# Optimization experiments

Measured on AMD Instinct MI355X. Metric: run time of the kernel, lower is better.

Reference implementation:

```python
import jax, jax.numpy as jnp
import numpy as np

N_NODES = 100000
N_EDGES = 1600000
EMB_DIM = 128
BN_EPS = 1e-5


def setup_inputs() -> dict:
    key = jax.random.key(0)
    k = jax.random.split(key, 5)
    x = jax.random.normal(k[0], (N_NODES, EMB_DIM), dtype=jnp.float32)
    src = jax.random.randint(k[1], (N_EDGES,), 0, N_NODES)
    dst = jax.random.randint(k[2], (N_EDGES,), 0, N_NODES)
    W = jax.random.normal(k[3], (EMB_DIM, EMB_DIM), dtype=jnp.float32) / np.float32(np.sqrt(EMB_DIM))
    b = jnp.zeros((EMB_DIM,), dtype=jnp.float32)
    gamma = jnp.ones((EMB_DIM,), dtype=jnp.float32)
    beta = jnp.zeros((EMB_DIM,), dtype=jnp.float32)
    return {"x": x, "src": src, "dst": dst, "W": W, "b": b, "gamma": gamma, "beta": beta}


def reference(x, src, dst, W, b, gamma, beta):
    n = x.shape[0]
    ones = jnp.ones(src.shape, dtype=x.dtype)
    # DGL GraphConv norm='both': degrees clamped to min 1
    deg_out = jnp.maximum(jax.ops.segment_sum(ones, src, num_segments=n), 1.0)
    deg_in = jnp.maximum(jax.ops.segment_sum(ones, dst, num_segments=n), 1.0)
    norm_src = jax.lax.rsqrt(deg_out)  # [N]
    norm_dst = jax.lax.rsqrt(deg_in)   # [N]
    # W applied before aggregation (in_feats == out_feats path in DGL)
    h = (x * norm_src[:, None]) @ W                              # [N, D]
    agg = jax.ops.segment_sum(h[src], dst, num_segments=n)       # SpMM gather/scatter, [N, D]
    h = agg * norm_dst[:, None] + b                              # [N, D]
    # BatchNorm1d over nodes (training-mode batch stats, biased variance)
    mean = jnp.mean(h, axis=0)
    var = jnp.var(h, axis=0)
    h = (h - mean) * jax.lax.rsqrt(var + BN_EPS) * gamma + beta
    h = jax.nn.relu(h)
    # dropout: identity in eval-mode reference
    return h + x  # residual
```

## Files before the change

### kernel.cpp

```cpp
#include <hip/hip_runtime.h>
#include <hip/hip_bf16.h>

#define NN 100000
#define NE 1600000
#define D  128
#define BN_EPS 1e-5f

#define CB  782
#define NC  256
#define EPC (NE / NC)
#define NSLICE  2
#define SLICESZ 61600
#define SW      (SLICESZ / 4)
#define SCH     256
#define EPH (NE / SCH)

#define GB   ((NN + 63) / 64)
#define SMB  ((NSLICE * SW + 255) / 256)

typedef __attribute__((ext_vector_type(8))) short bf16x8;
typedef __attribute__((ext_vector_type(4))) float f32x4;

#define WLD 136

static __device__ __forceinline__ ushort f2bf(float f) {
    __hip_bfloat16 b = __float2bfloat16(f);
    return *reinterpret_cast<ushort*>(&b);
}
static __device__ __forceinline__ float bflo(unsigned v) {
    return __uint_as_float((v & 0xffffu) << 16);
}
static __device__ __forceinline__ float bfhi(unsigned v) {
    return __uint_as_float(v & 0xffff0000u);
}

__global__ __launch_bounds__(256) void k_front(const int* __restrict__ src,
                                               const int* __restrict__ dst,
                                               const float* __restrict__ W,
                                               ushort* __restrict__ WT,
                                               int* __restrict__ SP,
                                               int* __restrict__ P,
                                               float* __restrict__ stats) {
    __shared__ int hist[SW];
    __shared__ int dh[CB];
    const int t = threadIdx.x;
    const int s = blockIdx.x >> 8;
    const int c = blockIdx.x & 255;
    for (int i = t; i < SW; i += 256) hist[i] = 0;
    for (int i = t; i < CB; i += 256) dh[i] = 0;
    __syncthreads();

    const int lo = s * SLICESZ;
    const int base = c * EPH;
    for (int i = t; i < EPH; i += 256) {
        int k = src[base + i] - lo;
        if ((unsigned)k < (unsigned)SLICESZ)
            atomicAdd(&hist[k >> 2], 1 << ((k & 3) * 8));
    }
    if (s == 0) {
        for (int i = t; i < EPH; i += 256)
            atomicAdd(&dh[dst[base + i] >> 7], 1);
    }
    __syncthreads();

    int* outS = SP + (size_t)blockIdx.x * SW;
    for (int i = t; i < SW; i += 256) outS[i] = hist[i];
    if (s == 0)
        for (int i = t; i < CB; i += 256) P[i * NC + c] = dh[i];
    if (s == 1 && c < 64) {
        int i = c * 256 + t;
        int n = i >> 7, k2 = i & 127;
        WT[i] = f2bf(W[k2 * D + n]);
    }
    if (s == 1 && c == 64) stats[t] = 0.0f;
}

__global__ __launch_bounds__(256) void k_mid(int* __restrict__ P,
                                             int* __restrict__ bintotal,
                                             const int* __restrict__ SP,
                                             float* __restrict__ degout) {
    const int t = threadIdx.x;
    if (blockIdx.x < CB) {
        __shared__ int sh[NC];
        const int b = blockIdx.x;
        const int v = P[b * NC + t];
        sh[t] = v;
        __syncthreads();
        for (int off = 1; off < NC; off <<= 1) {
            int u = (t >= off) ? sh[t - off] : 0;
            __syncthreads();
            sh[t] += u;
            __syncthreads();
        }
        P[b * NC + t] = sh[t] - v;
        if (t == NC - 1) bintotal[b] = sh[t];
    } else {
        int w = (blockIdx.x - CB) * 256 + t;
        if (w >= NSLICE * SW) return;
        const int s = w / SW, wi = w - s * SW;
        const int n0 = s * SLICESZ + wi * 4;
        if (n0 >= NN) return;
        const int* col = SP + (size_t)s * SCH * SW + wi;
        int b0 = 0, b1 = 0, b2 = 0, b3 = 0;
#pragma unroll 8
        for (int c = 0; c < SCH; ++c) {
            unsigned v = (unsigned)col[(size_t)c * SW];
            b0 += v & 0xFF;
            b1 += (v >> 8) & 0xFF;
            b2 += (v >> 16) & 0xFF;
            b3 += (v >> 24);
        }
        degout[n0] = (float)b0;
        if (n0 + 1 < NN) degout[n0 + 1] = (float)b1;
        if (n0 + 2 < NN) degout[n0 + 2] = (float)b2;
        if (n0 + 3 < NN) degout[n0 + 3] = (float)b3;
    }
}

__global__ __launch_bounds__(256) void k_csg(const float* __restrict__ x,
                                             const float* __restrict__ degout,
                                             const ushort* __restrict__ WT,
                                             ushort* __restrict__ h,
                                             const int* __restrict__ dst,
                                             const int* __restrict__ src,
                                             const int* __restrict__ P,
                                             const int* __restrict__ bintotal,
                                             int* __restrict__ binbase,
                                             int* __restrict__ sedge) {
    __shared__ ushort Wl[D * WLD];
    __shared__ int part[256];
    __shared__ int bb[CB];
    __shared__ int cur[CB];
    const int t = threadIdx.x;

    if (blockIdx.x < GB) {
        for (int s = t; s < 2048; s += 256) {
            int row = s >> 4, slot = s & 15;
            uint4 v = *reinterpret_cast<const uint4*>(WT + row * D + slot * 8);
            *reinterpret_cast<uint4*>(&Wl[row * WLD + slot * 8]) = v;
        }
        __syncthreads();

        const int wave = t >> 6;
        const int lane = t & 63;
        const int m16  = lane & 15;
        const int kq   = lane >> 4;
        const int row  = blockIdx.x * 64 + wave * 16 + m16;
        const int rc   = row < NN ? row : NN - 1;

        const float nrm = rsqrtf(fmaxf(degout[rc], 1.0f));

        bf16x8 afrag[4];
        const float* xr = x + (size_t)rc * D + kq * 8;
#pragma unroll
        for (int kt = 0; kt < 4; ++kt) {
            f32x4 lo = *reinterpret_cast<const f32x4*>(xr + kt * 32);
            f32x4 hi = *reinterpret_cast<const f32x4*>(xr + kt * 32 + 4);
            union { bf16x8 v; ushort u[8]; } af;
#pragma unroll
            for (int j = 0; j < 4; ++j) {
                af.u[j]     = f2bf(lo[j] * nrm);
                af.u[4 + j] = f2bf(hi[j] * nrm);
            }
            afrag[kt] = af.v;
        }

        f32x4 acc[8];
#pragma unroll
        for (int nt = 0; nt < 8; ++nt) acc[nt] = (f32x4)(0.0f);

#pragma unroll
        for (int kt = 0; kt < 4; ++kt) {
#pragma unroll
            for (int nt = 0; nt < 8; ++nt) {
                int n = nt * 16 + m16;
                const bf16x8 bfrag = *reinterpret_cast<const bf16x8*>(
                    &Wl[n * WLD + kt * 32 + kq * 8]);
                acc[nt] = __builtin_amdgcn_mfma_f32_16x16x32_bf16(afrag[kt], bfrag, acc[nt], 0, 0, 0);
            }
        }

        const int orow = blockIdx.x * 64 + wave * 16 + kq * 4;
#pragma unroll
        for (int nt = 0; nt < 8; ++nt) {
#pragma unroll
            for (int r = 0; r < 4; ++r) {
                int rr = orow + r;
                if (rr < NN) h[(size_t)rr * D + nt * 16 + m16] = f2bf(acc[nt][r]);
            }
        }
    } else {
        const int c = blockIdx.x - GB;
        int val[4];
        int sum = 0;
#pragma unroll
        for (int j = 0; j < 4; ++j) {
            int idx = t * 4 + j;
            val[j] = (idx < CB) ? bintotal[idx] : 0;
            sum += val[j];
        }
        part[t] = sum;
        __syncthreads();
        for (int off = 1; off < 256; off <<= 1) {
            int u = (t >= off) ? part[t - off] : 0;
            __syncthreads();
            part[t] += u;
            __syncthreads();
        }
        int run = (t == 0) ? 0 : part[t - 1];
#pragma unroll
        for (int j = 0; j < 4; ++j) {
            int idx = t * 4 + j;
            if (idx < CB) bb[idx] = run;
            run += val[j];
        }
        __syncthreads();
        if (c == 0) {
            for (int i = t; i < CB; i += 256) binbase[i] = bb[i];
            if (t == 0) binbase[CB] = part[255];
        }
        for (int i = t; i < CB; i += 256) cur[i] = bb[i] + P[i * NC + c];
        __syncthreads();
        const int base = c * EPC;
        for (int i = t; i < EPC; i += 256) {
            int d = dst[base + i];
            int pos = atomicAdd(&cur[d >> 7], 1);
            sedge[pos] = src[base + i] | ((d & 127) << 17);
        }
    }
}

__global__ __launch_bounds__(256) void k_fine(const int* __restrict__ sedge,
                                              const int* __restrict__ binbase,
                                              int* __restrict__ ptr,
                                              int* __restrict__ esrc) {
    __shared__ int fh[128], fp[128], fcur[128];
    const int b = blockIdx.x;
    const int t = threadIdx.x;
    const int lo = binbase[b], hi = binbase[b + 1];
    if (t < 128) fh[t] = 0;
    __syncthreads();
    for (int i = lo + t; i < hi; i += 256)
        atomicAdd(&fh[(unsigned)sedge[i] >> 17], 1);
    __syncthreads();
    if (t < 128) fp[t] = fh[t];
    __syncthreads();
    for (int off = 1; off < 128; off <<= 1) {
        int u = (t < 128 && t >= off) ? fp[t - off] : 0;
        __syncthreads();
        if (t < 128) fp[t] += u;
        __syncthreads();
    }
    if (t < 128) {
        const int node = b * 128 + t;
        const int ex = fp[t] - fh[t];
        fcur[t] = ex;
        if (node < NN) {
            ptr[node] = lo + ex;
        } else if (node == NN) {
            ptr[NN] = lo + ex;
        }
    }
    __syncthreads();
    for (int i = lo + t; i < hi; i += 256) {
        unsigned v = (unsigned)sedge[i];
        int pos = atomicAdd(&fcur[v >> 17], 1);
        esrc[lo + pos] = v & 0x1FFFF;
    }
}

__global__ __launch_bounds__(256) void k_agg(const ushort* __restrict__ h,
                                             const int* __restrict__ ptr,
                                             const int* __restrict__ esrc,
                                             const float* __restrict__ b,
                                             ushort* __restrict__ h2) {
    const int node = blockIdx.x * 4 + (threadIdx.x >> 6);
    const int lane = threadIdx.x & 63;
    if (node >= NN) return;
    const int s0 = ptr[node];
    const int s1 = ptr[node + 1];
    const int eg = lane >> 4;
    const int cb = (lane & 15) * 8;

    float acc[8];
#pragma unroll
    for (int j = 0; j < 8; ++j) acc[j] = 0.0f;

    for (int i = s0; i < s1; i += 16) {
        int  idx[4];
        bool p[4];
        uint4 v[4];
#pragma unroll
        for (int u = 0; u < 4; ++u) {
            int ii = i + eg + 4 * u;
            p[u] = ii < s1;
            if (p[u]) idx[u] = esrc[ii];
        }
#pragma unroll
        for (int u = 0; u < 4; ++u)
            if (p[u]) v[u] = *reinterpret_cast<const uint4*>(h + (size_t)idx[u] * D + cb);
#pragma unroll
        for (int u = 0; u < 4; ++u) {
            if (p[u]) {
                acc[0] += bflo(v[u].x); acc[1] += bfhi(v[u].x);
                acc[2] += bflo(v[u].y); acc[3] += bfhi(v[u].y);
                acc[4] += bflo(v[u].z); acc[5] += bfhi(v[u].z);
                acc[6] += bflo(v[u].w); acc[7] += bfhi(v[u].w);
            }
        }
    }
#pragma unroll
    for (int j = 0; j < 8; ++j) {
        acc[j] += __shfl_xor(acc[j], 16, 64);
        acc[j] += __shfl_xor(acc[j], 32, 64);
    }
    if (eg == 0) {
        const float nrm = rsqrtf(fmaxf((float)(s1 - s0), 1.0f));
        uint4 o;
        unsigned w[4];
#pragma unroll
        for (int m = 0; m < 4; ++m) {
            float e0 = acc[2 * m]     * nrm + b[cb + 2 * m];
            float e1 = acc[2 * m + 1] * nrm + b[cb + 2 * m + 1];
            w[m] = (unsigned)f2bf(e0) | ((unsigned)f2bf(e1) << 16);
        }
        o.x = w[0]; o.y = w[1]; o.z = w[2]; o.w = w[3];
        *reinterpret_cast<uint4*>(h2 + (size_t)node * D + cb) = o;
    }
}

__global__ __launch_bounds__(256) void k_stats(const unsigned* __restrict__ h2u,
                                               float* __restrict__ stats) {
    __shared__ float red[4][256];
    const int t = threadIdx.x;
    float s1lo = 0.f, s1hi = 0.f, s2lo = 0.f, s2hi = 0.f;
    const int total = NN * (D / 2);
    const int stride = gridDim.x * 256;
    for (int i = blockIdx.x * 256 + t; i < total; i += stride) {
        unsigned v = h2u[i];
        float lo = bflo(v), hi = bfhi(v);
        s1lo += lo; s1hi += hi;
        s2lo += lo * lo; s2hi += hi * hi;
    }
    red[0][t] = s1lo; red[1][t] = s1hi; red[2][t] = s2lo; red[3][t] = s2hi;
    __syncthreads();
    if (t < 64) {
        const int c = t * 2;
        float a0 = red[0][t] + red[0][t + 64] + red[0][t + 128] + red[0][t + 192];
        float a1 = red[1][t] + red[1][t + 64] + red[1][t + 128] + red[1][t + 192];
        float q0 = red[2][t] + red[2][t + 64] + red[2][t + 128] + red[2][t + 192];
        float q1 = red[3][t] + red[3][t + 64] + red[3][t + 128] + red[3][t + 192];
        atomicAdd(&stats[c], a0);
        atomicAdd(&stats[c + 1], a1);
        atomicAdd(&stats[128 + c], q0);
        atomicAdd(&stats[128 + c + 1], q1);
    }
}

__global__ void k_final(const uint2* __restrict__ h2v, const float4* __restrict__ xv,
                        const float* __restrict__ gamma, const float* __restrict__ beta,
                        const float* __restrict__ stats, float4* __restrict__ outv) {
    const int i = blockIdx.x * 256 + threadIdx.x;
    const int total = NN * (D / 4);
    if (i >= total) return;
    const int c = (i & 31) * 4;
    const float inv_n = 1.0f / (float)NN;
    uint2 v = h2v[i];
    float4 xx = xv[i];
    float hv[4] = { bflo(v.x), bfhi(v.x), bflo(v.y), bfhi(v.y) };
    float xr[4] = { xx.x, xx.y, xx.z, xx.w };
    float o[4];
#pragma unroll
    for (int m = 0; m < 4; ++m) {
        float mean = stats[c + m] * inv_n;
        float var  = stats[128 + c + m] * inv_n - mean * mean;
        float t = (hv[m] - mean) * rsqrtf(var + BN_EPS) * gamma[c + m] + beta[c + m];
        o[m] = fmaxf(t, 0.0f) + xr[m];
    }
    float4 ov; ov.x = o[0]; ov.y = o[1]; ov.z = o[2]; ov.w = o[3];
    outv[i] = ov;
}

extern "C" void kernel_launch(void* const* d_in, const int* in_sizes, int n_in,
                              void* d_out, int out_size, void* d_ws, size_t ws_size,
                              hipStream_t stream) {
    const float* x     = (const float*)d_in[0];
    const int*   src   = (const int*)d_in[1];
    const int*   dst   = (const int*)d_in[2];
    const float* W     = (const float*)d_in[3];
    const float* b     = (const float*)d_in[4];
    const float* gamma = (const float*)d_in[5];
    const float* beta  = (const float*)d_in[6];
    float* out = (float*)d_out;

    float* ws     = (float*)d_ws;
    ushort* h2    = (ushort*)ws;
    float* degout = ws + (size_t)NN * D;
    float* stats  = degout + NN;
    int*   ptr    = (int*)(stats + 256);
    int*   esrc   = ptr + (NN + 1);
    ushort* WT    = (ushort*)(esrc + NE);

    int* sedge    = (int*)ws;
    int* SP       = sedge + NE;
    int* P        = SP + (size_t)NSLICE * SCH * SW;
    int* bintotal = P + (size_t)CB * NC;
    int* binbase  = bintotal + CB;

    ushort* h = (ushort*)d_out;

    k_front<<<NSLICE * SCH, 256, 0, stream>>>(src, dst, W, WT, SP, P, stats);
    k_mid<<<CB + SMB, 256, 0, stream>>>(P, bintotal, SP, degout);
    k_csg<<<GB + NC, 256, 0, stream>>>(x, degout, WT, h, dst, src, P, bintotal, binbase, sedge);
    k_fine<<<CB, 256, 0, stream>>>(sedge, binbase, ptr, esrc);
    k_agg<<<(NN + 3) / 4, 256, 0, stream>>>(h, ptr, esrc, b, h2);
    k_stats<<<1024, 256, 0, stream>>>((const unsigned*)h2, stats);
    k_final<<<(NN * (D / 4) + 255) / 256, 256, 0, stream>>>((const uint2*)h2, (const float4*)x,
                                                            gamma, beta, stats, (float4*)out);
}
```

Before: 224.9 us.

## Split aggregation over feature slices so each wave covers 32 edges per node

The SpMM aggregation kernel now splits the 128-wide feature dimension into 8 slices of 16 columns, one slice per block, with each wave processing two nodes. Within a wave, 32 edges are gathered in parallel with 32 bytes per edge instead of 4 edges with full 256-byte rows. The aim is more independent gathers in flight per wave, and likely better L2 locality because concurrent blocks touch only one column slice of h. The cost is that the index array and row pointers are reread 8 times, each gather is a short 32-byte segment, and the cross-lane reduction grows to five shuffle steps.

```diff
diff --git a/kernel.cpp b/kernel.cpp
--- a/kernel.cpp
+++ b/kernel.cpp
@@ -274,58 +274,52 @@
                                              const int* __restrict__ esrc,
                                              const float* __restrict__ b,
                                              ushort* __restrict__ h2) {
-    const int node = blockIdx.x * 4 + (threadIdx.x >> 6);
-    const int lane = threadIdx.x & 63;
-    if (node >= NN) return;
-    const int s0 = ptr[node];
-    const int s1 = ptr[node + 1];
-    const int eg = lane >> 4;
-    const int cb = (lane & 15) * 8;
-
-    float acc[8];
-#pragma unroll
-    for (int j = 0; j < 8; ++j) acc[j] = 0.0f;
-
-    for (int i = s0; i < s1; i += 16) {
-        int  idx[4];
-        bool p[4];
-        uint4 v[4];
-#pragma unroll
-        for (int u = 0; u < 4; ++u) {
-            int ii = i + eg + 4 * u;
-            p[u] = ii < s1;
-            if (p[u]) idx[u] = esrc[ii];
-        }
-#pragma unroll
-        for (int u = 0; u < 4; ++u)
-            if (p[u]) v[u] = *reinterpret_cast<const uint4*>(h + (size_t)idx[u] * D + cb);
-#pragma unroll
-        for (int u = 0; u < 4; ++u) {
-            if (p[u]) {
-                acc[0] += bflo(v[u].x); acc[1] += bfhi(v[u].x);
-                acc[2] += bflo(v[u].y); acc[3] += bfhi(v[u].y);
-                acc[4] += bflo(v[u].z); acc[5] += bfhi(v[u].z);
-                acc[6] += bflo(v[u].w); acc[7] += bfhi(v[u].w);
-            }
-        }
-    }
-#pragma unroll
-    for (int j = 0; j < 8; ++j) {
-        acc[j] += __shfl_xor(acc[j], 16, 64);
-        acc[j] += __shfl_xor(acc[j], 32, 64);
-    }
-    if (eg == 0) {
-        const float nrm = rsqrtf(fmaxf((float)(s1 - s0), 1.0f));
-        uint4 o;
-        unsigned w[4];
-#pragma unroll
-        for (int m = 0; m < 4; ++m) {
-            float e0 = acc[2 * m]     * nrm + b[cb + 2 * m];
-            float e1 = acc[2 * m + 1] * nrm + b[cb + 2 * m + 1];
-            w[m] = (unsigned)f2bf(e0) | ((unsigned)f2bf(e1) << 16);
-        }
-        o.x = w[0]; o.y = w[1]; o.z = w[2]; o.w = w[3];
-        *reinterpret_cast<uint4*>(h2 + (size_t)node * D + cb) = o;
+    const int slice = blockIdx.x & 7;
+    const int ng    = blockIdx.x >> 3;
+    const int wid   = threadIdx.x >> 6;
+    const int lane  = threadIdx.x & 63;
+    const int eg    = lane >> 1;
+    const int cw    = lane & 1;
+    const int cb    = slice * 16 + cw * 8;
+
+#pragma unroll
+    for (int rep = 0; rep < 2; ++rep) {
+        const int node = ng * 8 + rep * 4 + wid;
+        if (node < NN) {
+            const int s0 = ptr[node];
+            const int s1 = ptr[node + 1];
+            float acc[8];
+#pragma unroll
+            for (int j = 0; j < 8; ++j) acc[j] = 0.0f;
+            for (int i = s0 + eg; i < s1; i += 32) {
+                int idx = esrc[i];
+                uint4 v = *reinterpret_cast<const uint4*>(h + (size_t)idx * D + cb);
+                acc[0] += bflo(v.x); acc[1] += bfhi(v.x);
+                acc[2] += bflo(v.y); acc[3] += bfhi(v.y);
+                acc[4] += bflo(v.z); acc[5] += bfhi(v.z);
+                acc[6] += bflo(v.w); acc[7] += bfhi(v.w);
+            }
+#pragma unroll
+            for (int j = 0; j < 8; ++j) {
+                acc[j] += __shfl_xor(acc[j], 2, 64);
+                acc[j] += __shfl_xor(acc[j], 4, 64);
+                acc[j] += __shfl_xor(acc[j], 8, 64);
+                acc[j] += __shfl_xor(acc[j], 16, 64);
+                acc[j] += __shfl_xor(acc[j], 32, 64);
+            }
+            if (eg == 0) {
+                const float nrm = rsqrtf(fmaxf((float)(s1 - s0), 1.0f));
+                unsigned w[4];
+#pragma unroll
+                for (int m = 0; m < 4; ++m) {
+                    float e0 = acc[2 * m]     * nrm + b[cb + 2 * m];
+                    float e1 = acc[2 * m + 1] * nrm + b[cb + 2 * m + 1];
+                    w[m] = (unsigned)f2bf(e0) | ((unsigned)f2bf(e1) << 16);
+                }
+                uint4 o; o.x = w[0]; o.y = w[1]; o.z = w[2]; o.w = w[3];
+                *reinterpret_cast<uint4*>(h2 + (size_t)node * D + cb) = o;
+            }
+        }
     }
 }
 
@@ -413,7 +407,7 @@
     k_mid<<<CB + SMB, 256, 0, stream>>>(P, bintotal, SP, degout);
     k_csg<<<GB + NC, 256, 0, stream>>>(x, degout, WT, h, dst, src, P, bintotal, binbase, sedge);
     k_fine<<<CB, 256, 0, stream>>>(sedge, binbase, ptr, esrc);
-    k_agg<<<(NN + 3) / 4, 256, 0, stream>>>(h, ptr, esrc, b, h2);
+    k_agg<<<((NN + 7) / 8) * 8, 256, 0, stream>>>(h, ptr, esrc, b, h2);
     k_stats<<<1024, 256, 0, stream>>>((const unsigned*)h2, stats);
     k_final<<<(NN * (D / 4) + 255) / 256, 256, 0, stream>>>((const uint2*)h2, (const float4*)x,
                                                             gamma, beta, stats, (float4*)out);
```

New measurement: 488.9 us. +117.4%, slower.
